# Kernel tuning notes

Hardware: AMD Instinct MI355X
Metric: run time of the kernel (lower is better)

The kernel has to match this reference:

```python
import jax, jax.numpy as jnp
import numpy as np

B, F, CI, CO, R = 64, 128, 64, 64, 4


def setup_inputs() -> dict:
    key = jax.random.key(0)
    k1, k2 = jax.random.split(key)
    ll = jax.random.normal(k1, (B, F, CI, R), dtype=jnp.float32)
    # WeightedSum requires non-negative weights (no softmax normalization)
    weights = jax.random.uniform(k2, (F, CI, CO, R), dtype=jnp.float32)
    return {"ll": ll, "weights": weights}


def reference(ll, weights):
    # log_weights: log(w) where w > 0, else -inf (zero weights contribute nothing)
    neg_inf = jnp.asarray(-jnp.inf, dtype=weights.dtype)
    log_w = jnp.where(weights > 0, jnp.log(jnp.where(weights > 0, weights, 1.0)), neg_inf)
    # broadcast add: (b,f,ci,1,r) + (1,f,ci,co,r) -> (b,f,ci,co,r), logsumexp over ci
    weighted = ll[:, :, :, None, :] + log_w[None]
    return jax.nn.logsumexp(weighted, axis=2)  # (b, f, co, r)
```

## Files before the change

kernel.cpp:

```cpp
#include <hip/hip_runtime.h>
#include <math.h>

typedef __attribute__((ext_vector_type(8))) short short8;
typedef __attribute__((ext_vector_type(4))) float f32x4;

#define L2E 1.44269504088896340736f
#define LN2 0.69314718055994530942f

static __device__ __forceinline__ unsigned int bfr(float x) {
    union { float f; unsigned u; } v; v.f = x;
    return (v.u + 0x7fffu + ((v.u >> 16) & 1u)) >> 16;
}
static __device__ __forceinline__ unsigned int pk2(float lo, float hi) {
    return bfr(lo) | (bfr(hi) << 16);
}

__global__ __launch_bounds__(256, 2)
void ws_kernel(const float* __restrict__ ll,
               const float* __restrict__ wt,
               float* __restrict__ out)
{
    __shared__ unsigned short Elds[4 * 32 * 64];
    __shared__ unsigned short Wlds[4 * 32 * 64];

    const int t   = threadIdx.x;
    const int blk = blockIdx.x;
    const int f   = blk >> 2;
    const int b0  = ((blk >> 1) & 1) * 32;
    const int co0 = (blk & 1) * 32;

    char* Ebase = (char*)Elds;
    char* Wbase = (char*)Wlds;

    {
        const float4* llv = (const float4*)ll;
        const int c  = t & 31;
        const int bb = t >> 5;
        #pragma unroll
        for (int k = 0; k < 4; ++k) {
            const int b = bb + 8 * k;
            const size_t base = (size_t)(b0 + b) * 8192 + (size_t)f * 64 + 2 * c;
            float4 v0 = llv[base];
            float4 v1 = llv[base + 1];
            float e0x = exp2f(v0.x * L2E), e0y = exp2f(v0.y * L2E),
                  e0z = exp2f(v0.z * L2E), e0w = exp2f(v0.w * L2E);
            float e1x = exp2f(v1.x * L2E), e1y = exp2f(v1.y * L2E),
                  e1z = exp2f(v1.z * L2E), e1w = exp2f(v1.w * L2E);
            const int off = (c * 4) ^ ((b & 7) << 4);
            char* rowp = Ebase + b * 128 + off;
            *(unsigned*)(rowp)         = pk2(e0x, e1x);
            *(unsigned*)(rowp + 4096)  = pk2(e0y, e1y);
            *(unsigned*)(rowp + 8192)  = pk2(e0z, e1z);
            *(unsigned*)(rowp + 12288) = pk2(e0w, e1w);
        }
    }
    {
        const float4* wv = (const float4*)wt;
        const int j = t & 31;
        #pragma unroll
        for (int k = 0; k < 2; ++k) {
            const int cq = (t >> 5) + 8 * k;
            const size_t base = (size_t)f * 4096 + (size_t)(4 * cq) * 64 + co0 + j;
            float4 q0 = wv[base];
            float4 q1 = wv[base + 64];
            float4 q2 = wv[base + 128];
            float4 q3 = wv[base + 192];
            const int off = (cq * 8) ^ ((j & 7) << 4);
            char* rowp = Wbase + j * 128 + off;
            *(uint2*)(rowp)         = make_uint2(pk2(q0.x, q1.x), pk2(q2.x, q3.x));
            *(uint2*)(rowp + 4096)  = make_uint2(pk2(q0.y, q1.y), pk2(q2.y, q3.y));
            *(uint2*)(rowp + 8192)  = make_uint2(pk2(q0.z, q1.z), pk2(q2.z, q3.z));
            *(uint2*)(rowp + 12288) = make_uint2(pk2(q0.w, q1.w), pk2(q2.w, q3.w));
        }
    }
    __syncthreads();

    const int r  = t >> 6;
    const int l  = t & 63;
    const int lr = l & 15;
    const int lg = l >> 4;
    const char* Ep = Ebase + r * 4096;
    const char* Wp = Wbase + r * 4096;

    f32x4 acc[2][2] = {{{0.f,0.f,0.f,0.f},{0.f,0.f,0.f,0.f}},
                       {{0.f,0.f,0.f,0.f},{0.f,0.f,0.f,0.f}}};
    const int swz = (lr & 7) << 4;
    #pragma unroll
    for (int kt = 0; kt < 2; ++kt) {
        const int sb = ((kt * 4 + lg) * 16) ^ swz;
        short8 a0 = *(const short8*)(Ep + lr * 128 + sb);
        short8 a1 = *(const short8*)(Ep + (lr + 16) * 128 + sb);
        short8 w0 = *(const short8*)(Wp + lr * 128 + sb);
        short8 w1 = *(const short8*)(Wp + (lr + 16) * 128 + sb);
        acc[0][0] = __builtin_amdgcn_mfma_f32_16x16x32_bf16(a0, w0, acc[0][0], 0, 0, 0);
        acc[0][1] = __builtin_amdgcn_mfma_f32_16x16x32_bf16(a0, w1, acc[0][1], 0, 0, 0);
        acc[1][0] = __builtin_amdgcn_mfma_f32_16x16x32_bf16(a1, w0, acc[1][0], 0, 0, 0);
        acc[1][1] = __builtin_amdgcn_mfma_f32_16x16x32_bf16(a1, w1, acc[1][1], 0, 0, 0);
    }

    float* op = out + ((size_t)b0 * 128 + f) * 256 + (size_t)(co0 + lr) * 4 + r;
    #pragma unroll
    for (int mt = 0; mt < 2; ++mt) {
        #pragma unroll
        for (int v = 0; v < 4; ++v) {
            const size_t bl = (size_t)(mt * 16 + lg * 4 + v) * 32768;
            op[bl]      = __log2f(acc[mt][0][v]) * LN2;
            op[bl + 64] = __log2f(acc[mt][1][v]) * LN2;
        }
    }
}

extern "C" void kernel_launch(void* const* d_in, const int* in_sizes, int n_in,
                              void* d_out, int out_size, void* d_ws, size_t ws_size,
                              hipStream_t stream)
{
    const float* ll = (const float*)d_in[0];
    const float* wt = (const float*)d_in[1];
    float* out = (float*)d_out;
    hipLaunchKernelGGL(ws_kernel, dim3(512), dim3(256), 0, stream, ll, wt, out);
}
```

Baseline: 13.19 us.

## Halve batch tile per block and stage output through LDS for coalesced stores

Splits the batch dimension into 16-row tiles so the grid doubles to 1024 blocks, and raises the occupancy hint to four blocks per CU. Results are written into a padded LDS buffer that reuses the E tile storage, then stored to global memory as contiguous float4 rows instead of scattered scalar stores. This targets poor store coalescing and low parallelism. In exchange, each weight tile is loaded and converted by twice as many blocks, and two extra barriers are added.

```diff
diff --git a/kernel.cpp b/kernel.cpp
--- a/kernel.cpp
+++ b/kernel.cpp
@@ -15,18 +15,19 @@
     return bfr(lo) | (bfr(hi) << 16);
 }
 
-__global__ __launch_bounds__(256, 2)
+__global__ __launch_bounds__(256, 4)
 void ws_kernel(const float* __restrict__ ll,
                const float* __restrict__ wt,
                float* __restrict__ out)
 {
-    __shared__ unsigned short Elds[4 * 32 * 64];
+    __shared__ unsigned short Elds[4 * 16 * 64];
     __shared__ unsigned short Wlds[4 * 32 * 64];
+    float* Obuf = (float*)Elds;
 
     const int t   = threadIdx.x;
     const int blk = blockIdx.x;
-    const int f   = blk >> 2;
-    const int b0  = ((blk >> 1) & 1) * 32;
+    const int f   = blk >> 3;
+    const int b0  = ((blk >> 1) & 3) * 16;
     const int co0 = (blk & 1) * 32;
 
     char* Ebase = (char*)Elds;
@@ -37,7 +38,7 @@
         const int c  = t & 31;
         const int bb = t >> 5;
         #pragma unroll
-        for (int k = 0; k < 4; ++k) {
+        for (int k = 0; k < 2; ++k) {
             const int b = bb + 8 * k;
             const size_t base = (size_t)(b0 + b) * 8192 + (size_t)f * 64 + 2 * c;
             float4 v0 = llv[base];
@@ -48,10 +49,10 @@
                   e1z = exp2f(v1.z * L2E), e1w = exp2f(v1.w * L2E);
             const int off = (c * 4) ^ ((b & 7) << 4);
             char* rowp = Ebase + b * 128 + off;
-            *(unsigned*)(rowp)         = pk2(e0x, e1x);
-            *(unsigned*)(rowp + 4096)  = pk2(e0y, e1y);
-            *(unsigned*)(rowp + 8192)  = pk2(e0z, e1z);
-            *(unsigned*)(rowp + 12288) = pk2(e0w, e1w);
+            *(unsigned*)(rowp)        = pk2(e0x, e1x);
+            *(unsigned*)(rowp + 2048) = pk2(e0y, e1y);
+            *(unsigned*)(rowp + 4096) = pk2(e0z, e1z);
+            *(unsigned*)(rowp + 6144) = pk2(e0w, e1w);
         }
     }
     {
@@ -79,33 +80,42 @@
     const int l  = t & 63;
     const int lr = l & 15;
     const int lg = l >> 4;
-    const char* Ep = Ebase + r * 4096;
+    const char* Ep = Ebase + r * 2048;
     const char* Wp = Wbase + r * 4096;
 
-    f32x4 acc[2][2] = {{{0.f,0.f,0.f,0.f},{0.f,0.f,0.f,0.f}},
-                       {{0.f,0.f,0.f,0.f},{0.f,0.f,0.f,0.f}}};
+    f32x4 acc[2] = {{0.f,0.f,0.f,0.f},{0.f,0.f,0.f,0.f}};
     const int swz = (lr & 7) << 4;
     #pragma unroll
     for (int kt = 0; kt < 2; ++kt) {
         const int sb = ((kt * 4 + lg) * 16) ^ swz;
         short8 a0 = *(const short8*)(Ep + lr * 128 + sb);
-        short8 a1 = *(const short8*)(Ep + (lr + 16) * 128 + sb);
         short8 w0 = *(const short8*)(Wp + lr * 128 + sb);
         short8 w1 = *(const short8*)(Wp + (lr + 16) * 128 + sb);
-        acc[0][0] = __builtin_amdgcn_mfma_f32_16x16x32_bf16(a0, w0, acc[0][0], 0, 0, 0);
-        acc[0][1] = __builtin_amdgcn_mfma_f32_16x16x32_bf16(a0, w1, acc[0][1], 0, 0, 0);
-        acc[1][0] = __builtin_amdgcn_mfma_f32_16x16x32_bf16(a1, w0, acc[1][0], 0, 0, 0);
-        acc[1][1] = __builtin_amdgcn_mfma_f32_16x16x32_bf16(a1, w1, acc[1][1], 0, 0, 0);
+        acc[0] = __builtin_amdgcn_mfma_f32_16x16x32_bf16(a0, w0, acc[0], 0, 0, 0);
+        acc[1] = __builtin_amdgcn_mfma_f32_16x16x32_bf16(a0, w1, acc[1], 0, 0, 0);
     }
 
-    float* op = out + ((size_t)b0 * 128 + f) * 256 + (size_t)(co0 + lr) * 4 + r;
+    __syncthreads();
+
     #pragma unroll
-    for (int mt = 0; mt < 2; ++mt) {
+    for (int nt = 0; nt < 2; ++nt) {
         #pragma unroll
         for (int v = 0; v < 4; ++v) {
-            const size_t bl = (size_t)(mt * 16 + lg * 4 + v) * 32768;
-            op[bl]      = __log2f(acc[mt][0][v]) * LN2;
-            op[bl + 64] = __log2f(acc[mt][1][v]) * LN2;
+            Obuf[(lg * 4 + v) * 132 + (nt * 16 + lr) * 4 + r] =
+                __log2f(acc[nt][v]) * LN2;
+        }
+    }
+    __syncthreads();
+
+    {
+        const int row  = t >> 5;
+        const int j    = t & 31;
+        #pragma unroll
+        for (int k = 0; k < 2; ++k) {
+            const int b = row + 8 * k;
+            float4 v = *(const float4*)&Obuf[b * 132 + j * 4];
+            float* op = out + ((size_t)(b0 + b) * 128 + f) * 256 + (size_t)co0 * 4;
+            *(float4*)(op + j * 4) = v;
         }
     }
 }
@@ -117,5 +127,5 @@
     const float* ll = (const float*)d_in[0];
     const float* wt = (const float*)d_in[1];
     float* out = (float*)d_out;
-    hipLaunchKernelGGL(ws_kernel, dim3(512), dim3(256), 0, stream, ll, wt, out);
+    hipLaunchKernelGGL(ws_kernel, dim3(1024), dim3(256), 0, stream, ll, wt, out);
 }
```

After: 14.66 us. +11.1%, slower.
